# Kernel tuning notes

Hardware: AMD Instinct MI355X
Metric: run time of the kernel (lower is better)

Reference implementation:

```python
import jax, jax.numpy as jnp
import numpy as np

N, LQ, LK, D, H = 2, 2048, 2048, 1024, 16


def setup_inputs() -> dict:
    root = jax.random.key(0)
    k0, k1, k2, k3, k4 = jax.random.split(root, 5)
    s = 1.0 / np.float32(np.sqrt(D))  # fan-in init scale for Linear weights
    query = jax.random.normal(k0, (N, LQ, D), jnp.float32)
    key = jax.random.normal(k1, (N, LK, D), jnp.float32)
    Wq = jax.random.normal(k2, (D, D), jnp.float32) * s
    Wk = jax.random.normal(k3, (D, D), jnp.float32) * s
    Wv = jax.random.normal(k4, (D, D), jnp.float32) * s
    # causal mask: True above the diagonal => attention set to -inf
    mask = jnp.triu(jnp.ones((LQ, LK), dtype=bool), k=1)
    # padding mask: per-sentence valid key lengths (tail is padding)
    lengths = jnp.array([LK, LK - 256], dtype=jnp.int32)  # (N,)
    padding_mask = jnp.arange(LK)[None, :] >= lengths[:, None]  # (N, LK) bool
    return {"query": query, "key": key, "Wq": Wq, "Wk": Wk, "Wv": Wv,
            "mask": mask, "padding_mask": padding_mask, "n_heads": H}


def reference(query, key, Wq, Wk, Wv, mask, padding_mask, n_heads):
    n, lq, d_model = query.shape
    lk = key.shape[1]
    h = n_heads
    d = d_model // h
    # torch Linear: y = x @ W^T  (no bias)
    q = (query @ Wq.T).reshape(n, lq, h, d).transpose(0, 2, 1, 3)  # (N,H,Lq,d)
    k = (key @ Wk.T).reshape(n, lk, h, d).transpose(0, 2, 1, 3)    # (N,H,Lk,d)
    v = (key @ Wv.T).reshape(n, lk, h, d).transpose(0, 2, 1, 3)    # (N,H,Lk,d)
    # non-standard scaling: sqrt of the number of valid (non-padded) keys per sentence
    valid = jnp.sum((~padding_mask).astype(q.dtype), axis=-1)      # (N,)
    scaling = jnp.sqrt(valid)[:, None, None, None]                 # (N,1,1,1)
    score = jnp.einsum('nhqd,nhkd->nhqk', q, k) / scaling          # (N,H,Lq,Lk)
    full_mask = mask[None, None, :, :] | padding_mask[:, None, None, :]
    score = jnp.where(full_mask, -jnp.inf, score)
    p = jax.nn.softmax(score, axis=-1)
    attn = jnp.einsum('nhqk,nhkd->nhqd', p, v)                     # (N,H,Lq,d)
    return attn.transpose(0, 2, 1, 3).reshape(n, lq, d_model)
```

## Files before the change

### kernel.cpp

```cpp
#include <hip/hip_runtime.h>
#include <math.h>

typedef __attribute__((ext_vector_type(8))) short short8;
typedef __attribute__((ext_vector_type(4))) float f32x4;

#define NB 2
#define LQ 2048
#define LK 2048
#define DM 1024
#define NH 16
#define HD 64

__device__ __forceinline__ unsigned short f2bf(float f) {
    unsigned u = __builtin_bit_cast(unsigned, f);
    u = (u + 0x7FFFu + ((u >> 16) & 1u)) >> 16;
    return (unsigned short)u;
}

__device__ __forceinline__ void gload16(const void* g, void* l) {
    __builtin_amdgcn_global_load_lds(
        (const __attribute__((address_space(1))) void*)g,
        (__attribute__((address_space(3))) void*)l, 16, 0, 0);
}

__device__ __forceinline__ unsigned cvtpk(float a, float b) {
    unsigned r;
    asm("v_cvt_pk_bf16_f32 %0, %1, %2" : "=v"(r) : "v"(a), "v"(b));
    return r;
}

__device__ __forceinline__ short8 lds_load8(const unsigned short* base, int row, int col) {
    int byte = (row * 128 + col * 2) ^ ((row & 7) << 4);
    return *(const short8*)((const char*)base + byte);
}

__global__ __launch_bounds__(256) void convertk(
    const float* __restrict__ q, const float* __restrict__ k,
    const float* __restrict__ wq, const float* __restrict__ wk,
    const float* __restrict__ wv, unsigned short* __restrict__ dst)
{
    long i4 = (long)blockIdx.x * 256 + threadIdx.x;
    long e = i4 * 4;
    if (e >= 11534336L) return;
    const float* src; long off;
    if (e < 4194304L)       { src = q;  off = e; }
    else if (e < 8388608L)  { src = k;  off = e - 4194304L; }
    else if (e < 9437184L)  { src = wq; off = e - 8388608L; }
    else if (e < 10485760L) { src = wk; off = e - 9437184L; }
    else                    { src = wv; off = e - 10485760L; }
    float4 v = *(const float4*)(src + off);
    ushort4 r;
    r.x = f2bf(v.x); r.y = f2bf(v.y); r.z = f2bf(v.z); r.w = f2bf(v.w);
    *(ushort4*)(dst + e) = r;
}

__global__ __launch_bounds__(256) void scalek(const unsigned char* __restrict__ pm,
                                              float* __restrict__ scal, int* __restrict__ vlen)
{
    __shared__ int red[256];
    int t = threadIdx.x;
    for (int n = 0; n < NB; n++) {
        int cnt = 0;
        for (int i = t; i < LK; i += 256) cnt += (pm[n * LK + i] == 0) ? 1 : 0;
        red[t] = cnt;
        __syncthreads();
        for (int s = 128; s > 0; s >>= 1) {
            if (t < s) red[t] += red[t + s];
            __syncthreads();
        }
        if (t == 0) { vlen[n] = red[0]; scal[n] = 1.0f / sqrtf((float)red[0]); }
        __syncthreads();
    }
}

__global__ __launch_bounds__(256) void gemm3(
    const unsigned short* __restrict__ Qb, const unsigned short* __restrict__ Kb,
    const unsigned short* __restrict__ Wqb, const unsigned short* __restrict__ Wkb,
    const unsigned short* __restrict__ Wvb,
    unsigned short* __restrict__ Qp, unsigned short* __restrict__ Kp, unsigned short* __restrict__ Vp)
{
    const unsigned short *A, *B;
    unsigned short* C;
    int z = blockIdx.z;
    if (z == 0)      { A = Qb; B = Wqb; C = Qp; }
    else if (z == 1) { A = Kb; B = Wkb; C = Kp; }
    else             { A = Kb; B = Wvb; C = Vp; }
    const int K = DM, NN = DM;
    __shared__ unsigned short As[4096];
    __shared__ unsigned short Bs[4096];
    int t = threadIdx.x, wave = t >> 6, lane = t & 63;
    int bm = blockIdx.x * 128, bn = blockIdx.y * 128;
    int wr = (wave >> 1) * 64, wc = (wave & 1) * 64;
    int sr = wave * 16 + (lane >> 2);
    int sc = (lane & 3) * 8;
    int frow = lane & 15, fk = (lane >> 4) * 8;
    f32x4 zero = {0.f, 0.f, 0.f, 0.f};
    f32x4 acc[4][4];
    for (int i = 0; i < 4; i++) for (int j = 0; j < 4; j++) acc[i][j] = zero;

    for (int k0 = 0; k0 < K; k0 += 32) {
        const unsigned short* a0 = A + (size_t)(bm + sr) * K + k0 + sc;
        const unsigned short* b0 = B + (size_t)(bn + sr) * K + k0 + sc;
        gload16(a0, &As[wave * 512]);
        gload16(a0 + (size_t)64 * K, &As[2048 + wave * 512]);
        gload16(b0, &Bs[wave * 512]);
        gload16(b0 + (size_t)64 * K, &Bs[2048 + wave * 512]);
        __syncthreads();
        short8 af[4], bfr[4];
#pragma unroll
        for (int i = 0; i < 4; i++) af[i]  = *(const short8*)&As[(wr + i * 16 + frow) * 32 + fk];
#pragma unroll
        for (int j = 0; j < 4; j++) bfr[j] = *(const short8*)&Bs[(wc + j * 16 + frow) * 32 + fk];
#pragma unroll
        for (int i = 0; i < 4; i++)
#pragma unroll
            for (int j = 0; j < 4; j++)
                acc[i][j] = __builtin_amdgcn_mfma_f32_16x16x32_bf16(af[i], bfr[j], acc[i][j], 0, 0, 0);
        __syncthreads();
    }
    int ccol = lane & 15, crow = (lane >> 4) * 4;
#pragma unroll
    for (int i = 0; i < 4; i++)
#pragma unroll
        for (int j = 0; j < 4; j++) {
            int col = bn + wc + j * 16 + ccol;
#pragma unroll
            for (int r = 0; r < 4; r++) {
                int row = bm + wr + i * 16 + crow + r;
                C[(size_t)row * NN + col] = f2bf(acc[i][j][r]);
            }
        }
}

__global__ __launch_bounds__(256) void transposek(const unsigned short* __restrict__ V,
                                                  unsigned short* __restrict__ Vt)
{
    __shared__ unsigned short tile[64][65];
    int n = blockIdx.z;
    int k0 = blockIdx.x * 64, d0 = blockIdx.y * 64;
    int t = threadIdx.x;
#pragma unroll
    for (int it = 0; it < 2; it++) {
        int r = (t >> 3) + it * 32, c = (t & 7) * 8;
        short8 v = *(const short8*)&V[((size_t)(n * LK + k0 + r)) * DM + d0 + c];
#pragma unroll
        for (int j = 0; j < 8; j++) tile[r][c + j] = (unsigned short)v[j];
    }
    __syncthreads();
#pragma unroll
    for (int it = 0; it < 2; it++) {
        int r2 = (t >> 3) + it * 32, c2 = (t & 7) * 8;
        short8 v;
#pragma unroll
        for (int j = 0; j < 8; j++) v[j] = (short)tile[c2 + j][r2];
        *(short8*)&Vt[((size_t)(n * DM + d0 + r2)) * LK + k0 + c2] = v;
    }
}


__device__ __forceinline__ void stage_kv(const unsigned short* Kp, const unsigned short* Vt,
    unsigned short* KsB, unsigned short* VsB, int n, int h, int k0, int w, int srl, int scs)
{
#pragma unroll
    for (int i = 0; i < 4; i++) {
        int row = 8 * w + 16 * i + srl;
        gload16(Kp + (size_t)(n * LK + k0 + row) * DM + h * HD + scs, KsB + w * 512 + i * 1024);
        gload16(Vt + (size_t)(n * DM + h * HD + row) * LK + k0 + scs, VsB + w * 512 + i * 1024);
    }
}

__device__ __forceinline__ void attn_phase(
    const short8 (&kf)[4][2], const unsigned short* VsCur, unsigned short* PsW,
    const short8& qf0, const short8& qf1,
    int qw, int k0, int vlen, float c2,
    f32x4 (&o)[4], float& m_run, float& l_run, int lane)
{
    const int c = lane & 15, g = lane >> 4;
    const int fk = g * 8;
    f32x4 zero = {0.f, 0.f, 0.f, 0.f};
    f32x4 sv[4];
#pragma unroll
    for (int kt = 0; kt < 4; kt++) {
        f32x4 z = zero;
        z = __builtin_amdgcn_mfma_f32_16x16x32_bf16(kf[kt][0], qf0, z, 0, 0, 0);
        z = __builtin_amdgcn_mfma_f32_16x16x32_bf16(kf[kt][1], qf1, z, 0, 0, 0);
        sv[kt] = z;
    }
    bool full = (k0 + 63 <= qw) && (k0 + 64 <= vlen);
    if (!full) {
        int q = qw + c;
#pragma unroll
        for (int kt = 0; kt < 4; kt++)
#pragma unroll
            for (int r = 0; r < 4; r++) {
                int kg = k0 + kt * 16 + g * 4 + r;
                if (kg > q || kg >= vlen) sv[kt][r] = -INFINITY;
            }
    }
    float mx = fmaxf(fmaxf(sv[0][0], sv[0][1]), fmaxf(sv[0][2], sv[0][3]));
#pragma unroll
    for (int kt = 1; kt < 4; kt++)
        mx = fmaxf(mx, fmaxf(fmaxf(sv[kt][0], sv[kt][1]), fmaxf(sv[kt][2], sv[kt][3])));
    mx = fmaxf(mx, __shfl_xor(mx, 16));
    mx = fmaxf(mx, __shfl_xor(mx, 32));
    float mn = fmaxf(m_run, mx);
    float al = __builtin_amdgcn_exp2f((m_run - mn) * c2);
    float ssum = 0.f;
#pragma unroll
    for (int kt = 0; kt < 4; kt++)
#pragma unroll
        for (int r = 0; r < 4; r++) {
            float p = __builtin_amdgcn_exp2f((sv[kt][r] - mn) * c2);
            sv[kt][r] = p;
            ssum += p;
        }
    ssum += __shfl_xor(ssum, 16);
    ssum += __shfl_xor(ssum, 32);
    l_run = l_run * al + ssum;
    m_run = mn;
    float alr[4];
#pragma unroll
    for (int r = 0; r < 4; r++) alr[r] = __shfl(al, 4 * g + r);
#pragma unroll
    for (int dt = 0; dt < 4; dt++)
#pragma unroll
        for (int r = 0; r < 4; r++) o[dt][r] *= alr[r];
#pragma unroll
    for (int kt = 0; kt < 4; kt++) {
        uint2 pw;
        pw.x = cvtpk(sv[kt][0], sv[kt][1]);
        pw.y = cvtpk(sv[kt][2], sv[kt][3]);
        int byte = (c * 128 + (kt * 16 + g * 4) * 2) ^ ((c & 7) << 4);
        *(uint2*)((char*)PsW + byte) = pw;
    }
#pragma unroll
    for (int ks = 0; ks < 2; ks++) {
        short8 ap = lds_load8(PsW, c, ks * 32 + fk);
#pragma unroll
        for (int dt = 0; dt < 4; dt++) {
            short8 bv = lds_load8(VsCur, dt * 16 + c, ks * 32 + fk);
            o[dt] = __builtin_amdgcn_mfma_f32_16x16x32_bf16(ap, bv, o[dt], 0, 0, 0);
        }
    }
}

__device__ __forceinline__ void attn_epilogue(float* out, const f32x4 (&o)[4], float l_run,
                                              int n, int h, int qw, int lane)
{
    int c = lane & 15, g = lane >> 4;
    float lr[4];
#pragma unroll
    for (int r = 0; r < 4; r++) lr[r] = __shfl(l_run, 4 * g + r);
#pragma unroll
    for (int dt = 0; dt < 4; dt++)
#pragma unroll
        for (int r = 0; r < 4; r++) {
            int q = qw + 4 * g + r;
            int d = h * HD + dt * 16 + c;
            out[((size_t)n * LQ + q) * DM + d] = o[dt][r] / lr[r];
        }
}

__global__ __launch_bounds__(128, 2) void attnk(
    const unsigned short* __restrict__ Qp, const unsigned short* __restrict__ Kp,
    const unsigned short* __restrict__ Vt,
    const float* __restrict__ scal, const int* __restrict__ vlenp,
    float* __restrict__ out)
{
    __shared__ unsigned short Ks[2][4096];
    __shared__ unsigned short Vs[2][4096];
    __shared__ unsigned short Ps[2][2][1024];
    int t = threadIdx.x, w = t >> 6, lane = t & 63;
    int bid = blockIdx.x;
    int r3 = bid >> 8;
    int xs = ((bid >> 3) + (r3 << 3)) & 31;
    int y  = (bid & 7) * 4 + r3;
    int n = y >> 4, h = y & 15;
    int qwA = xs * 32 + 16 * w;
    int qwB = (63 - xs) * 32 + 16 * w;
    float c2 = scal[n] * 1.4426950408889634f;
    int vlen = vlenp[n];
    int kvt = (vlen + 63) >> 6;
    int ntA = min((xs >> 1) + 1, kvt);
    int ntB = min(((63 - xs) >> 1) + 1, kvt);
    int frow = lane & 15, fk = (lane >> 4) * 8;
    int srl = lane >> 3;
    int scs = ((lane & 7) ^ srl) << 3;

    const unsigned short* qA = Qp + (size_t)(n * LQ + qwA + frow) * DM + h * HD;
    const unsigned short* qB = Qp + (size_t)(n * LQ + qwB + frow) * DM + h * HD;
    short8 qA0 = *(const short8*)(qA + fk), qA1 = *(const short8*)(qA + 32 + fk);
    short8 qB0 = *(const short8*)(qB + fk), qB1 = *(const short8*)(qB + 32 + fk);

    stage_kv(Kp, Vt, Ks[0], Vs[0], n, h, 0, w, srl, scs);
    __syncthreads();

    f32x4 zero = {0.f, 0.f, 0.f, 0.f};
    f32x4 oA[4] = {zero, zero, zero, zero};
    f32x4 oB[4] = {zero, zero, zero, zero};
    float mA = -INFINITY, lA = 0.f, mB = -INFINITY, lB = 0.f;

    int ti = 0;
    for (; ti < ntA; ti++) {
        int cur = ti & 1, k0 = ti * 64;
        if (ti + 1 < ntB) stage_kv(Kp, Vt, Ks[cur ^ 1], Vs[cur ^ 1], n, h, k0 + 64, w, srl, scs);
        short8 kf[4][2];
#pragma unroll
        for (int kt = 0; kt < 4; kt++) {
            kf[kt][0] = lds_load8(Ks[cur], kt * 16 + frow, fk);
            kf[kt][1] = lds_load8(Ks[cur], kt * 16 + frow, 32 + fk);
        }
        attn_phase(kf, Vs[cur], &Ps[w][0][0], qA0, qA1, qwA, k0, vlen, c2, oA, mA, lA, lane);
        attn_phase(kf, Vs[cur], &Ps[w][1][0], qB0, qB1, qwB, k0, vlen, c2, oB, mB, lB, lane);
        __syncthreads();
    }
    attn_epilogue(out, oA, lA, n, h, qwA, lane);
    for (; ti < ntB; ti++) {
        int cur = ti & 1, k0 = ti * 64;
        if (ti + 1 < ntB) stage_kv(Kp, Vt, Ks[cur ^ 1], Vs[cur ^ 1], n, h, k0 + 64, w, srl, scs);
        short8 kf[4][2];
#pragma unroll
        for (int kt = 0; kt < 4; kt++) {
            kf[kt][0] = lds_load8(Ks[cur], kt * 16 + frow, fk);
            kf[kt][1] = lds_load8(Ks[cur], kt * 16 + frow, 32 + fk);
        }
        attn_phase(kf, Vs[cur], &Ps[w][1][0], qB0, qB1, qwB, k0, vlen, c2, oB, mB, lB, lane);
        __syncthreads();
    }
    attn_epilogue(out, oB, lB, n, h, qwB, lane);
}

extern "C" void kernel_launch(void* const* d_in, const int* in_sizes, int n_in,
                              void* d_out, int out_size, void* d_ws, size_t ws_size,
                              hipStream_t stream) {
    const float* query = (const float*)d_in[0];
    const float* key   = (const float*)d_in[1];
    const float* Wq    = (const float*)d_in[2];
    const float* Wk    = (const float*)d_in[3];
    const float* Wv    = (const float*)d_in[4];
    const unsigned char* pmask = (const unsigned char*)d_in[6];
    float* out = (float*)d_out;

    char* ws = (char*)d_ws;
    unsigned short* bfbase = (unsigned short*)ws;
    unsigned short* Qb  = bfbase;
    unsigned short* Kb  = bfbase + 4194304L;
    unsigned short* Wqb = bfbase + 8388608L;
    unsigned short* Wkb = bfbase + 9437184L;
    unsigned short* Wvb = bfbase + 10485760L;
    unsigned short* Qp  = (unsigned short*)(ws + 23068672L);
    unsigned short* Kp  = (unsigned short*)(ws + 31457280L);
    unsigned short* Vp  = (unsigned short*)(ws + 39845888L);
    unsigned short* Vt  = (unsigned short*)(ws + 48234496L);
    float* scal = (float*)(ws + 56623104L);
    int*   vlen = (int*)(ws + 56623104L + 64);

    convertk<<<11264, 256, 0, stream>>>(query, key, Wq, Wk, Wv, bfbase);
    scalek<<<1, 256, 0, stream>>>(pmask, scal, vlen);
    gemm3<<<dim3(32, 8, 3), 256, 0, stream>>>(Qb, Kb, Wqb, Wkb, Wvb, Qp, Kp, Vp);
    transposek<<<dim3(32, 16, 2), 256, 0, stream>>>(Vp, Vt);
    attnk<<<1024, 128, 0, stream>>>(Qp, Kp, Vt, scal, vlen, out);
}
```

Before: 197.8 us.

## Rework GEMM k-tiling, fuse mask reduction, stream KV directly in attention

The projection GEMM now stages 64-wide k-slices with an XOR-swizzled LDS layout, which halves the barrier count per K. The padding-length reduction kernel is removed and each attention block computes the valid length itself with popcounts and wave shuffles. The attention kernel drops shared K/V staging and double buffering and reads K and V fragments straight from global memory (relying on cache), merges the A/B query loops, and adds s_setprio around the MFMA sections. It also adds a lazy rescale of the online softmax, skipping the rescale unless the max grows by more than a threshold, and raises occupancy to 3 blocks. Global K/V reads may cost more bandwidth and latency than the LDS-staged version, and the lazy rescale may change numerical behaviour slightly.

```diff
diff --git a/kernel.cpp b/kernel.cpp
--- a/kernel.cpp
+++ b/kernel.cpp
@@ -54,25 +54,6 @@
     *(ushort4*)(dst + e) = r;
 }
 
-__global__ __launch_bounds__(256) void scalek(const unsigned char* __restrict__ pm,
-                                              float* __restrict__ scal, int* __restrict__ vlen)
-{
-    __shared__ int red[256];
-    int t = threadIdx.x;
-    for (int n = 0; n < NB; n++) {
-        int cnt = 0;
-        for (int i = t; i < LK; i += 256) cnt += (pm[n * LK + i] == 0) ? 1 : 0;
-        red[t] = cnt;
-        __syncthreads();
-        for (int s = 128; s > 0; s >>= 1) {
-            if (t < s) red[t] += red[t + s];
-            __syncthreads();
-        }
-        if (t == 0) { vlen[n] = red[0]; scal[n] = 1.0f / sqrtf((float)red[0]); }
-        __syncthreads();
-    }
-}
-
 __global__ __launch_bounds__(256) void gemm3(
     const unsigned short* __restrict__ Qb, const unsigned short* __restrict__ Kb,
     const unsigned short* __restrict__ Wqb, const unsigned short* __restrict__ Wkb,
@@ -86,36 +67,39 @@
     else if (z == 1) { A = Kb; B = Wkb; C = Kp; }
     else             { A = Kb; B = Wvb; C = Vp; }
     const int K = DM, NN = DM;
-    __shared__ unsigned short As[4096];
-    __shared__ unsigned short Bs[4096];
+    __shared__ unsigned short As[8192];
+    __shared__ unsigned short Bs[8192];
     int t = threadIdx.x, wave = t >> 6, lane = t & 63;
     int bm = blockIdx.x * 128, bn = blockIdx.y * 128;
     int wr = (wave >> 1) * 64, wc = (wave & 1) * 64;
-    int sr = wave * 16 + (lane >> 2);
-    int sc = (lane & 3) * 8;
+    int srow = lane >> 3;
+    int scol = ((lane & 7) << 3) ^ (srow << 3);
     int frow = lane & 15, fk = (lane >> 4) * 8;
     f32x4 zero = {0.f, 0.f, 0.f, 0.f};
     f32x4 acc[4][4];
     for (int i = 0; i < 4; i++) for (int j = 0; j < 4; j++) acc[i][j] = zero;
 
-    for (int k0 = 0; k0 < K; k0 += 32) {
-        const unsigned short* a0 = A + (size_t)(bm + sr) * K + k0 + sc;
-        const unsigned short* b0 = B + (size_t)(bn + sr) * K + k0 + sc;
-        gload16(a0, &As[wave * 512]);
-        gload16(a0 + (size_t)64 * K, &As[2048 + wave * 512]);
-        gload16(b0, &Bs[wave * 512]);
-        gload16(b0 + (size_t)64 * K, &Bs[2048 + wave * 512]);
+    for (int k0 = 0; k0 < K; k0 += 64) {
+#pragma unroll
+        for (int i = 0; i < 4; i++) {
+            int r0 = wave * 32 + i * 8;
+            gload16(A + (size_t)(bm + r0 + srow) * K + k0 + scol, &As[r0 * 64]);
+            gload16(B + (size_t)(bn + r0 + srow) * K + k0 + scol, &Bs[r0 * 64]);
+        }
         __syncthreads();
-        short8 af[4], bfr[4];
-#pragma unroll
-        for (int i = 0; i < 4; i++) af[i]  = *(const short8*)&As[(wr + i * 16 + frow) * 32 + fk];
-#pragma unroll
-        for (int j = 0; j < 4; j++) bfr[j] = *(const short8*)&Bs[(wc + j * 16 + frow) * 32 + fk];
-#pragma unroll
-        for (int i = 0; i < 4; i++)
-#pragma unroll
-            for (int j = 0; j < 4; j++)
-                acc[i][j] = __builtin_amdgcn_mfma_f32_16x16x32_bf16(af[i], bfr[j], acc[i][j], 0, 0, 0);
+#pragma unroll
+        for (int half = 0; half < 2; half++) {
+            short8 af[4], bfr[4];
+#pragma unroll
+            for (int i = 0; i < 4; i++) af[i]  = lds_load8(As, wr + i * 16 + frow, half * 32 + fk);
+#pragma unroll
+            for (int j = 0; j < 4; j++) bfr[j] = lds_load8(Bs, wc + j * 16 + frow, half * 32 + fk);
+#pragma unroll
+            for (int i = 0; i < 4; i++)
+#pragma unroll
+                for (int j = 0; j < 4; j++)
+                    acc[i][j] = __builtin_amdgcn_mfma_f32_16x16x32_bf16(af[i], bfr[j], acc[i][j], 0, 0, 0);
+        }
         __syncthreads();
     }
     int ccol = lane & 15, crow = (lane >> 4) * 4;
@@ -158,34 +142,12 @@
 }
 
 
-__device__ __forceinline__ void stage_kv(const unsigned short* Kp, const unsigned short* Vt,
-    unsigned short* KsB, unsigned short* VsB, int n, int h, int k0, int w, int srl, int scs)
-{
-#pragma unroll
-    for (int i = 0; i < 4; i++) {
-        int row = 8 * w + 16 * i + srl;
-        gload16(Kp + (size_t)(n * LK + k0 + row) * DM + h * HD + scs, KsB + w * 512 + i * 1024);
-        gload16(Vt + (size_t)(n * DM + h * HD + row) * LK + k0 + scs, VsB + w * 512 + i * 1024);
-    }
-}
-
-__device__ __forceinline__ void attn_phase(
-    const short8 (&kf)[4][2], const unsigned short* VsCur, unsigned short* PsW,
-    const short8& qf0, const short8& qf1,
+__device__ __forceinline__ void softmax_pack(
+    f32x4 (&sv)[4], unsigned short* PsW,
     int qw, int k0, int vlen, float c2,
     f32x4 (&o)[4], float& m_run, float& l_run, int lane)
 {
     const int c = lane & 15, g = lane >> 4;
-    const int fk = g * 8;
-    f32x4 zero = {0.f, 0.f, 0.f, 0.f};
-    f32x4 sv[4];
-#pragma unroll
-    for (int kt = 0; kt < 4; kt++) {
-        f32x4 z = zero;
-        z = __builtin_amdgcn_mfma_f32_16x16x32_bf16(kf[kt][0], qf0, z, 0, 0, 0);
-        z = __builtin_amdgcn_mfma_f32_16x16x32_bf16(kf[kt][1], qf1, z, 0, 0, 0);
-        sv[kt] = z;
-    }
     bool full = (k0 + 63 <= qw) && (k0 + 64 <= vlen);
     if (!full) {
         int q = qw + c;
@@ -203,28 +165,31 @@
         mx = fmaxf(mx, fmaxf(fmaxf(sv[kt][0], sv[kt][1]), fmaxf(sv[kt][2], sv[kt][3])));
     mx = fmaxf(mx, __shfl_xor(mx, 16));
     mx = fmaxf(mx, __shfl_xor(mx, 32));
-    float mn = fmaxf(m_run, mx);
-    float al = __builtin_amdgcn_exp2f((m_run - mn) * c2);
+    if (__any((mx - m_run) * c2 > 8.0f)) {
+        float mn = fmaxf(m_run, mx);
+        float al = __builtin_amdgcn_exp2f((m_run - mn) * c2);
+        float alr[4];
+#pragma unroll
+        for (int r = 0; r < 4; r++) alr[r] = __shfl(al, 4 * g + r);
+#pragma unroll
+        for (int dt = 0; dt < 4; dt++)
+#pragma unroll
+            for (int r = 0; r < 4; r++) o[dt][r] *= alr[r];
+        l_run *= al;
+        m_run = mn;
+    }
     float ssum = 0.f;
 #pragma unroll
     for (int kt = 0; kt < 4; kt++)
 #pragma unroll
         for (int r = 0; r < 4; r++) {
-            float p = __builtin_amdgcn_exp2f((sv[kt][r] - mn) * c2);
+            float p = __builtin_amdgcn_exp2f((sv[kt][r] - m_run) * c2);
             sv[kt][r] = p;
             ssum += p;
         }
     ssum += __shfl_xor(ssum, 16);
     ssum += __shfl_xor(ssum, 32);
-    l_run = l_run * al + ssum;
-    m_run = mn;
-    float alr[4];
-#pragma unroll
-    for (int r = 0; r < 4; r++) alr[r] = __shfl(al, 4 * g + r);
-#pragma unroll
-    for (int dt = 0; dt < 4; dt++)
-#pragma unroll
-        for (int r = 0; r < 4; r++) o[dt][r] *= alr[r];
+    l_run += ssum;
 #pragma unroll
     for (int kt = 0; kt < 4; kt++) {
         uint2 pw;
@@ -233,15 +198,6 @@
         int byte = (c * 128 + (kt * 16 + g * 4) * 2) ^ ((c & 7) << 4);
         *(uint2*)((char*)PsW + byte) = pw;
     }
-#pragma unroll
-    for (int ks = 0; ks < 2; ks++) {
-        short8 ap = lds_load8(PsW, c, ks * 32 + fk);
-#pragma unroll
-        for (int dt = 0; dt < 4; dt++) {
-            short8 bv = lds_load8(VsCur, dt * 16 + c, ks * 32 + fk);
-            o[dt] = __builtin_amdgcn_mfma_f32_16x16x32_bf16(ap, bv, o[dt], 0, 0, 0);
-        }
-    }
 }
 
 __device__ __forceinline__ void attn_epilogue(float* out, const f32x4 (&o)[4], float l_run,
@@ -261,14 +217,11 @@
         }
 }
 
-__global__ __launch_bounds__(128, 2) void attnk(
+__global__ __launch_bounds__(128, 3) void attnk(
     const unsigned short* __restrict__ Qp, const unsigned short* __restrict__ Kp,
-    const unsigned short* __restrict__ Vt,
-    const float* __restrict__ scal, const int* __restrict__ vlenp,
+    const unsigned short* __restrict__ Vt, const unsigned char* __restrict__ pm,
     float* __restrict__ out)
 {
-    __shared__ unsigned short Ks[2][4096];
-    __shared__ unsigned short Vs[2][4096];
     __shared__ unsigned short Ps[2][2][1024];
     int t = threadIdx.x, w = t >> 6, lane = t & 63;
     int bid = blockIdx.x;
@@ -278,55 +231,82 @@
     int n = y >> 4, h = y & 15;
     int qwA = xs * 32 + 16 * w;
     int qwB = (63 - xs) * 32 + 16 * w;
-    float c2 = scal[n] * 1.4426950408889634f;
-    int vlen = vlenp[n];
+    const int c = lane & 15, g = lane >> 4, fk = g * 8;
+
+    int vlen;
+    {
+        const uint4* pmv = (const uint4*)(pm + (size_t)n * LK);
+        uint4 a = pmv[lane * 2], b = pmv[lane * 2 + 1];
+        int ones = __popc(a.x) + __popc(a.y) + __popc(a.z) + __popc(a.w)
+                 + __popc(b.x) + __popc(b.y) + __popc(b.z) + __popc(b.w);
+        int zeros = 32 - ones;
+#pragma unroll
+        for (int off = 1; off < 64; off <<= 1) zeros += __shfl_xor(zeros, off);
+        vlen = zeros;
+    }
+    float c2 = 1.4426950408889634f / sqrtf((float)vlen);
     int kvt = (vlen + 63) >> 6;
     int ntA = min((xs >> 1) + 1, kvt);
     int ntB = min(((63 - xs) >> 1) + 1, kvt);
-    int frow = lane & 15, fk = (lane >> 4) * 8;
-    int srl = lane >> 3;
-    int scs = ((lane & 7) ^ srl) << 3;
-
-    const unsigned short* qA = Qp + (size_t)(n * LQ + qwA + frow) * DM + h * HD;
-    const unsigned short* qB = Qp + (size_t)(n * LQ + qwB + frow) * DM + h * HD;
+
+    const unsigned short* Kbase = Kp + (size_t)n * LK * DM + h * HD;
+    const unsigned short* Vbase = Vt + ((size_t)n * DM + h * HD) * LK;
+
+    const unsigned short* qA = Qp + (size_t)(n * LQ + qwA + c) * DM + h * HD;
+    const unsigned short* qB = Qp + (size_t)(n * LQ + qwB + c) * DM + h * HD;
     short8 qA0 = *(const short8*)(qA + fk), qA1 = *(const short8*)(qA + 32 + fk);
     short8 qB0 = *(const short8*)(qB + fk), qB1 = *(const short8*)(qB + 32 + fk);
-
-    stage_kv(Kp, Vt, Ks[0], Vs[0], n, h, 0, w, srl, scs);
-    __syncthreads();
 
     f32x4 zero = {0.f, 0.f, 0.f, 0.f};
     f32x4 oA[4] = {zero, zero, zero, zero};
     f32x4 oB[4] = {zero, zero, zero, zero};
     float mA = -INFINITY, lA = 0.f, mB = -INFINITY, lB = 0.f;
-
-    int ti = 0;
-    for (; ti < ntA; ti++) {
-        int cur = ti & 1, k0 = ti * 64;
-        if (ti + 1 < ntB) stage_kv(Kp, Vt, Ks[cur ^ 1], Vs[cur ^ 1], n, h, k0 + 64, w, srl, scs);
-        short8 kf[4][2];
+    unsigned short* PsA = &Ps[w][0][0];
+    unsigned short* PsB = &Ps[w][1][0];
+
+    for (int ti = 0; ti < ntB; ti++) {
+        int k0 = ti * 64;
+        bool doA = ti < ntA;
+        const unsigned short* Kt = Kbase + (size_t)k0 * DM;
+        f32x4 svA[4], svB[4];
+        __builtin_amdgcn_s_setprio(1);
 #pragma unroll
         for (int kt = 0; kt < 4; kt++) {
-            kf[kt][0] = lds_load8(Ks[cur], kt * 16 + frow, fk);
-            kf[kt][1] = lds_load8(Ks[cur], kt * 16 + frow, 32 + fk);
-        }
-        attn_phase(kf, Vs[cur], &Ps[w][0][0], qA0, qA1, qwA, k0, vlen, c2, oA, mA, lA, lane);
-        attn_phase(kf, Vs[cur], &Ps[w][1][0], qB0, qB1, qwB, k0, vlen, c2, oB, mB, lB, lane);
-        __syncthreads();
+            const unsigned short* kr = Kt + (size_t)(kt * 16 + c) * DM;
+            short8 kf0 = *(const short8*)(kr + fk);
+            short8 kf1 = *(const short8*)(kr + 32 + fk);
+            f32x4 zB = zero;
+            zB = __builtin_amdgcn_mfma_f32_16x16x32_bf16(kf0, qB0, zB, 0, 0, 0);
+            zB = __builtin_amdgcn_mfma_f32_16x16x32_bf16(kf1, qB1, zB, 0, 0, 0);
+            svB[kt] = zB;
+            if (doA) {
+                f32x4 zA = zero;
+                zA = __builtin_amdgcn_mfma_f32_16x16x32_bf16(kf0, qA0, zA, 0, 0, 0);
+                zA = __builtin_amdgcn_mfma_f32_16x16x32_bf16(kf1, qA1, zA, 0, 0, 0);
+                svA[kt] = zA;
+            }
+        }
+        __builtin_amdgcn_s_setprio(0);
+
+        if (doA) softmax_pack(svA, PsA, qwA, k0, vlen, c2, oA, mA, lA, lane);
+        softmax_pack(svB, PsB, qwB, k0, vlen, c2, oB, mB, lB, lane);
+
+        __builtin_amdgcn_s_setprio(1);
+#pragma unroll
+        for (int ks = 0; ks < 2; ks++) {
+            short8 apB = lds_load8(PsB, c, ks * 32 + fk);
+            short8 apA;
+            if (doA) apA = lds_load8(PsA, c, ks * 32 + fk);
+#pragma unroll
+            for (int dt = 0; dt < 4; dt++) {
+                short8 bv = *(const short8*)(Vbase + (size_t)(dt * 16 + c) * LK + k0 + ks * 32 + fk);
+                oB[dt] = __builtin_amdgcn_mfma_f32_16x16x32_bf16(apB, bv, oB[dt], 0, 0, 0);
+                if (doA) oA[dt] = __builtin_amdgcn_mfma_f32_16x16x32_bf16(apA, bv, oA[dt], 0, 0, 0);
+            }
+        }
+        __builtin_amdgcn_s_setprio(0);
     }
     attn_epilogue(out, oA, lA, n, h, qwA, lane);
-    for (; ti < ntB; ti++) {
-        int cur = ti & 1, k0 = ti * 64;
-        if (ti + 1 < ntB) stage_kv(Kp, Vt, Ks[cur ^ 1], Vs[cur ^ 1], n, h, k0 + 64, w, srl, scs);
-        short8 kf[4][2];
-#pragma unroll
-        for (int kt = 0; kt < 4; kt++) {
-            kf[kt][0] = lds_load8(Ks[cur], kt * 16 + frow, fk);
-            kf[kt][1] = lds_load8(Ks[cur], kt * 16 + frow, 32 + fk);
-        }
-        attn_phase(kf, Vs[cur], &Ps[w][1][0], qB0, qB1, qwB, k0, vlen, c2, oB, mB, lB, lane);
-        __syncthreads();
-    }
     attn_epilogue(out, oB, lB, n, h, qwB, lane);
 }
 
@@ -352,12 +332,9 @@
     unsigned short* Kp  = (unsigned short*)(ws + 31457280L);
     unsigned short* Vp  = (unsigned short*)(ws + 39845888L);
     unsigned short* Vt  = (unsigned short*)(ws + 48234496L);
-    float* scal = (float*)(ws + 56623104L);
-    int*   vlen = (int*)(ws + 56623104L + 64);
 
     convertk<<<11264, 256, 0, stream>>>(query, key, Wq, Wk, Wv, bfbase);
-    scalek<<<1, 256, 0, stream>>>(pmask, scal, vlen);
     gemm3<<<dim3(32, 8, 3), 256, 0, stream>>>(Qb, Kb, Wqb, Wkb, Wvb, Qp, Kp, Vp);
     transposek<<<dim3(32, 16, 2), 256, 0, stream>>>(Vp, Vt);
-    attnk<<<1024, 128, 0, stream>>>(Qp, Kp, Vt, scal, vlen, out);
-}
+    attnk<<<1024, 128, 0, stream>>>(Qp, Kp, Vt, pmask, out);
+}
```

New measurement: 269.0 us. 36.0% more time.
